# Performance work log

Measured on AMD Instinct MI355X. Metric: run time of the kernel, lower is better.

## Reference

```python
import jax, jax.numpy as jnp
import numpy as np

N_NODES = 50000
N_EDGES = 800000
N_GRAPHS = 128
ORIG_FEA = 92
NBR_FEA = 41
H = 64
N_CONV = 3
BN_EPS = 1e-5


def setup_inputs() -> dict:
    key = jax.random.key(0)
    ks = jax.random.split(key, 16)
    x = jax.random.normal(ks[0], (N_NODES, ORIG_FEA), dtype=jnp.float32)
    edge_attr = jax.random.normal(ks[1], (N_EDGES, NBR_FEA), dtype=jnp.float32)
    edge_index = jax.random.randint(ks[2], (2, N_EDGES), 0, N_NODES)
    batch = jnp.sort(jax.random.randint(ks[3], (N_NODES,), 0, N_GRAPHS))
    s_emb1 = 1.0 / np.sqrt(ORIG_FEA)
    s_emb2 = 1.0 / np.sqrt(NBR_FEA)
    s_conv = 1.0 / np.sqrt(3 * H)
    s_h = 1.0 / np.sqrt(H)
    return {
        "x": x,
        "edge_attr": edge_attr,
        "edge_index": edge_index,
        "batch": batch,
        "W_emb1": jax.random.uniform(ks[4], (ORIG_FEA, H), jnp.float32, -s_emb1, s_emb1),
        "b_emb1": jnp.zeros((H,), jnp.float32),
        "W_emb2": jax.random.uniform(ks[5], (NBR_FEA, H), jnp.float32, -s_emb2, s_emb2),
        "b_emb2": jnp.zeros((H,), jnp.float32),
        "Wf": jax.random.uniform(ks[6], (N_CONV, 3 * H, H), jnp.float32, -s_conv, s_conv),
        "bf": jnp.zeros((N_CONV, H), jnp.float32),
        "Ws": jax.random.uniform(ks[7], (N_CONV, 3 * H, H), jnp.float32, -s_conv, s_conv),
        "bs": jnp.zeros((N_CONV, H), jnp.float32),
        "gamma": jnp.ones((N_CONV, H), jnp.float32),
        "beta": jnp.zeros((N_CONV, H), jnp.float32),
        "W1": jax.random.uniform(ks[8], (H, H), jnp.float32, -s_h, s_h),
        "b1": jnp.zeros((H,), jnp.float32),
        "W2": jax.random.uniform(ks[9], (H, H), jnp.float32, -s_h, s_h),
        "b2": jnp.zeros((H,), jnp.float32),
        "Wo": jax.random.uniform(ks[10], (H, 1), jnp.float32, -s_h, s_h),
        "bo": jnp.zeros((1,), jnp.float32),
    }


def _batch_norm(h, g, b):
    # training-mode BatchNorm1d: biased batch statistics
    mu = jnp.mean(h, axis=0)
    var = jnp.var(h, axis=0)
    return (h - mu) * jax.lax.rsqrt(var + BN_EPS) * g + b


def reference(x, edge_attr, edge_index, batch, W_emb1, b_emb1, W_emb2, b_emb2,
              Wf, bf, Ws, bs, gamma, beta, W1, b1, W2, b2, Wo, bo):
    src = edge_index[0]  # x_j (source)
    dst = edge_index[1]  # x_i (target, aggregation index)
    h = x @ W_emb1 + b_emb1              # [N, H]
    e = edge_attr @ W_emb2 + b_emb2      # [E, H]
    for a in range(N_CONV):
        # CGConv: z_ij = [x_i, x_j, e_ij]; msg = sigmoid(lin_f(z)) * softplus(lin_s(z))
        z = jnp.concatenate([h[dst], h[src], e], axis=1)       # [E, 3H]
        msg = jax.nn.sigmoid(z @ Wf[a] + bf[a]) * jax.nn.softplus(z @ Ws[a] + bs[a])
        h = h + jax.ops.segment_sum(msg, dst, num_segments=N_NODES)
        h = _batch_norm(h, gamma[a], beta[a])
        if a != N_CONV - 1:
            h = jax.nn.relu(h)
        # dropout ratio is 0 -> no-op
    # JK='last' -> node representation is final h; mean pooling per graph
    sums = jax.ops.segment_sum(h, batch, num_segments=N_GRAPHS)              # [G, H]
    cnts = jax.ops.segment_sum(jnp.ones((N_NODES,), h.dtype), batch, num_segments=N_GRAPHS)
    y = sums / jnp.maximum(cnts, 1.0)[:, None]
    y = jax.nn.softplus(y @ W1 + b1)
    y = jax.nn.softplus(y @ W2 + b2)
    y = (y @ Wo + bo).squeeze(-1)  # [G]
    return y
```

## Files before the change

### kernel.cpp

```cpp
#include <hip/hip_runtime.h>
#include <hip/hip_bf16.h>
#include <math.h>

#define N_NODES 50000
#define N_EDGES 800000
#define N_GRAPHS 128
#define ORIG_FEA 92
#define NBR_FEA 41
#define H 64
#define N_CONV 3
#define BN_EPS 1e-5f

typedef float v2f __attribute__((ext_vector_type(2)));

__device__ __forceinline__ float sigmoidf_(float x) {
    return __fdividef(1.f, 1.f + __expf(-x));
}
__device__ __forceinline__ float softplusf_(float x) {
    return fmaxf(x, 0.f) + __logf(1.f + __expf(-fabsf(x)));
}

__global__ __launch_bounds__(256) void fold_kernel(
    const float* __restrict__ W_emb2, const float* __restrict__ b_emb2,
    const float* __restrict__ Wf, const float* __restrict__ bf,
    const float* __restrict__ Ws, const float* __restrict__ bs,
    float* __restrict__ W2c, float* __restrict__ cfs) {
    int a = blockIdx.x >> 1, gate = blockIdx.x & 1;
    const float* W = (gate ? Ws : Wf) + a * 192 * H + 128 * H;
    const float* bias = (gate ? bs : bf) + a * H;
    float* Wout = W2c + a * NBR_FEA * 2 * H;
    float* cout = cfs + a * 2 * H;
    for (int idx = threadIdx.x; idx < NBR_FEA * H; idx += blockDim.x) {
        int k = idx / H, j = idx % H;
        float acc = 0.f;
        for (int m = 0; m < H; ++m) acc += W_emb2[k * H + m] * W[m * H + j];
        Wout[k * 2 * H + 2 * j + gate] = acc;
    }
    for (int j = threadIdx.x; j < H; j += blockDim.x) {
        float acc = bias[j];
        for (int m = 0; m < H; ++m) acc += b_emb2[m] * W[m * H + j];
        cout[2 * j + gate] = acc;
    }
}

__global__ __launch_bounds__(256) void embed_kernel(
    const float* __restrict__ x, const float* __restrict__ W,
    const float* __restrict__ b, float* __restrict__ h) {
    __shared__ float lw[ORIG_FEA * H];
    for (int i = threadIdx.x; i < ORIG_FEA * H; i += blockDim.x) lw[i] = W[i];
    __syncthreads();
    int lane = threadIdx.x & 63;
    int wid = (blockIdx.x * blockDim.x + threadIdx.x) >> 6;
    int nw = (gridDim.x * blockDim.x) >> 6;
    for (int n = wid; n < N_NODES; n += nw) {
        int nu = __builtin_amdgcn_readfirstlane(n);
        const float* xr = x + (size_t)nu * ORIG_FEA;
        float acc = b[lane];
#pragma unroll
        for (int k = 0; k < ORIG_FEA; ++k) acc += xr[k] * lw[k * H + lane];
        h[(size_t)nu * H + lane] = acc;
    }
}

__global__ __launch_bounds__(256) void node_proj_kernel(
    const float* __restrict__ h,
    const float* __restrict__ Wf, const float* __restrict__ Ws,
    float* __restrict__ NPi, float* __restrict__ NPj,
    float* __restrict__ hsum) {
    __shared__ float lw[4 * H * H];
    for (int i = threadIdx.x; i < H * H; i += blockDim.x) {
        lw[i] = Wf[i];
        lw[H * H + i] = Wf[H * H + i];
        lw[2 * H * H + i] = Ws[i];
        lw[3 * H * H + i] = Ws[H * H + i];
    }
    __syncthreads();
    int lane = threadIdx.x & 63;
    int wid = (blockIdx.x * blockDim.x + threadIdx.x) >> 6;
    int nw = (gridDim.x * blockDim.x) >> 6;
    for (int n = wid; n < N_NODES; n += nw) {
        int nu = __builtin_amdgcn_readfirstlane(n);
        const float* hr = h + (size_t)nu * H;
        float pf = 0.f, qf = 0.f, ps = 0.f, qs = 0.f;
#pragma unroll
        for (int k = 0; k < H; ++k) {
            float s = hr[k];
            pf += s * lw[k * H + lane];
            qf += s * lw[H * H + k * H + lane];
            ps += s * lw[2 * H * H + k * H + lane];
            qs += s * lw[3 * H * H + k * H + lane];
        }
        v2f pi; pi.x = pf; pi.y = ps;
        v2f pj; pj.x = qf; pj.y = qs;
        *(v2f*)&NPi[(size_t)nu * 2 * H + 2 * lane] = pi;
        *(v2f*)&NPj[(size_t)nu * 2 * H + 2 * lane] = pj;
        hsum[(size_t)nu * H + lane] = hr[lane];
    }
}

__global__ __launch_bounds__(256, 2) void edge_kernel(
    const int* __restrict__ ei, const float* __restrict__ ea,
    const float* __restrict__ NPi, const float* __restrict__ NPj,
    const float* __restrict__ W2c, const float* __restrict__ cfs,
    float* __restrict__ hsum) {
    int lane = threadIdx.x & 63;
    v2f w[NBR_FEA];
#pragma unroll
    for (int k = 0; k < NBR_FEA; ++k)
        w[k] = *(const v2f*)&W2c[k * 2 * H + 2 * lane];
    v2f c2 = *(const v2f*)&cfs[2 * lane];
#pragma unroll
    for (int k = 0; k < NBR_FEA; ++k) asm volatile("" : "+v"(w[k]));
    int wid = (blockIdx.x * blockDim.x + threadIdx.x) >> 6;
    int nw = (gridDim.x * blockDim.x) >> 6;
    for (int e = wid; e < N_EDGES; e += nw) {
        int eu = __builtin_amdgcn_readfirstlane(e);
        int src = ei[eu];
        int dst = ei[N_EDGES + eu];
        v2f pi = *(const v2f*)&NPi[(size_t)dst * 2 * H + 2 * lane];
        v2f pj = *(const v2f*)&NPj[(size_t)src * 2 * H + 2 * lane];
        v2f acc = c2 + pi + pj;
        const float* er = ea + (size_t)eu * NBR_FEA;
#pragma unroll
        for (int k = 0; k < NBR_FEA; ++k) acc += w[k] * er[k];
        float msg = sigmoidf_(acc.x) * softplusf_(acc.y);
        atomicAdd(&hsum[(size_t)dst * H + lane], msg);
    }
}

__global__ __launch_bounds__(256) void bn_stats_kernel(
    const float* __restrict__ hsum, float* __restrict__ stats) {
    int lane = threadIdx.x & 63;
    int wl = threadIdx.x >> 6;
    int wid = (blockIdx.x * blockDim.x + threadIdx.x) >> 6;
    int nw = (gridDim.x * blockDim.x) >> 6;
    float s = 0.f, s2 = 0.f;
    for (int n = wid; n < N_NODES; n += nw) {
        float v = hsum[(size_t)n * H + lane];
        s += v;
        s2 += v * v;
    }
    __shared__ float ls[4 * 2 * H];
    ls[wl * 2 * H + lane] = s;
    ls[wl * 2 * H + H + lane] = s2;
    __syncthreads();
    if (wl == 0) {
        float a = ls[lane] + ls[2 * H + lane] + ls[4 * H + lane] + ls[6 * H + lane];
        float b = ls[H + lane] + ls[3 * H + lane] + ls[5 * H + lane] + ls[7 * H + lane];
        atomicAdd(&stats[lane], a);
        atomicAdd(&stats[H + lane], b);
    }
}

__global__ __launch_bounds__(256) void bn_apply_kernel(
    const float* __restrict__ hsum, const float* __restrict__ stats,
    const float* __restrict__ gamma, const float* __restrict__ beta,
    float* __restrict__ h, int relu) {
    int idx0 = blockIdx.x * blockDim.x + threadIdx.x;
    int stride = gridDim.x * blockDim.x;
    const float inv_n = 1.f / (float)N_NODES;
    for (int idx = idx0; idx < N_NODES * H; idx += stride) {
        int j = idx & (H - 1);
        float mu = stats[j] * inv_n;
        float var = stats[H + j] * inv_n - mu * mu;
        float inv = rsqrtf(var + BN_EPS);
        float v = (hsum[idx] - mu) * inv * gamma[j] + beta[j];
        if (relu) v = fmaxf(v, 0.f);
        h[idx] = v;
    }
}

__global__ __launch_bounds__(256) void pool_kernel(
    const float* __restrict__ h, const int* __restrict__ batch,
    float* __restrict__ gsum, float* __restrict__ gcnt) {
    int lane = threadIdx.x & 63;
    int wid = (blockIdx.x * blockDim.x + threadIdx.x) >> 6;
    int nw = (gridDim.x * blockDim.x) >> 6;
    for (int n = wid; n < N_NODES; n += nw) {
        int nu = __builtin_amdgcn_readfirstlane(n);
        int g = batch[nu];
        atomicAdd(&gsum[(size_t)g * H + lane], h[(size_t)nu * H + lane]);
        if (lane == 0) atomicAdd(&gcnt[g], 1.f);
    }
}

__global__ __launch_bounds__(64) void mlp_kernel(
    const float* __restrict__ gsum, const float* __restrict__ gcnt,
    const float* __restrict__ W1, const float* __restrict__ b1,
    const float* __restrict__ W2, const float* __restrict__ b2,
    const float* __restrict__ Wo, const float* __restrict__ bo,
    float* __restrict__ out) {
    int g = blockIdx.x;
    int lane = threadIdx.x;
    __shared__ float y[H];
    float cnt = fmaxf(gcnt[g], 1.f);
    y[lane] = gsum[(size_t)g * H + lane] / cnt;
    __syncthreads();
    float acc = b1[lane];
#pragma unroll
    for (int k = 0; k < H; ++k) acc += y[k] * W1[k * H + lane];
    float y1 = softplusf_(acc);
    __syncthreads();
    y[lane] = y1;
    __syncthreads();
    acc = b2[lane];
#pragma unroll
    for (int k = 0; k < H; ++k) acc += y[k] * W2[k * H + lane];
    float y2 = softplusf_(acc);
    float t = y2 * Wo[lane];
#pragma unroll
    for (int o = 32; o > 0; o >>= 1) t += __shfl_down(t, o, 64);
    if (lane == 0) out[g] = t + bo[0];
}

extern "C" void kernel_launch(void* const* d_in, const int* in_sizes, int n_in,
                              void* d_out, int out_size, void* d_ws, size_t ws_size,
                              hipStream_t stream) {
    const float* x = (const float*)d_in[0];
    const float* ea = (const float*)d_in[1];
    const int* ei = (const int*)d_in[2];
    const int* batch = (const int*)d_in[3];
    const float* W_emb1 = (const float*)d_in[4];
    const float* b_emb1 = (const float*)d_in[5];
    const float* W_emb2 = (const float*)d_in[6];
    const float* b_emb2 = (const float*)d_in[7];
    const float* Wf = (const float*)d_in[8];
    const float* bf = (const float*)d_in[9];
    const float* Ws = (const float*)d_in[10];
    const float* bs = (const float*)d_in[11];
    const float* gamma = (const float*)d_in[12];
    const float* beta = (const float*)d_in[13];
    const float* W1 = (const float*)d_in[14];
    const float* b1 = (const float*)d_in[15];
    const float* W2 = (const float*)d_in[16];
    const float* b2 = (const float*)d_in[17];
    const float* Wo = (const float*)d_in[18];
    const float* bo = (const float*)d_in[19];
    float* out = (float*)d_out;

    float* w = (float*)d_ws;
    float* stats = w;
    float* gsum = w + 3 * 2 * H;
    float* gcnt = gsum + N_GRAPHS * H;
    float* h = gcnt + N_GRAPHS;
    float* hsum = h + (size_t)N_NODES * H;
    float* NPi = hsum + (size_t)N_NODES * H;
    float* NPj = NPi + (size_t)N_NODES * 2 * H;
    float* W2c = NPj + (size_t)N_NODES * 2 * H;
    float* cfs = W2c + 3 * NBR_FEA * 2 * H;

    hipMemsetAsync(w, 0, (3 * 2 * H + N_GRAPHS * H + N_GRAPHS) * sizeof(float), stream);

    fold_kernel<<<6, 256, 0, stream>>>(W_emb2, b_emb2, Wf, bf, Ws, bs, W2c, cfs);
    embed_kernel<<<512, 256, 0, stream>>>(x, W_emb1, b_emb1, h);

    for (int a = 0; a < N_CONV; ++a) {
        node_proj_kernel<<<512, 256, 0, stream>>>(h, Wf + a * 192 * H, Ws + a * 192 * H,
                                                  NPi, NPj, hsum);
        edge_kernel<<<2048, 256, 0, stream>>>(ei, ea, NPi, NPj,
                                              W2c + a * NBR_FEA * 2 * H,
                                              cfs + a * 2 * H, hsum);
        bn_stats_kernel<<<256, 256, 0, stream>>>(hsum, stats + a * 2 * H);
        bn_apply_kernel<<<2048, 256, 0, stream>>>(hsum, stats + a * 2 * H,
                                                  gamma + a * H, beta + a * H, h,
                                                  a != N_CONV - 1 ? 1 : 0);
    }

    pool_kernel<<<784, 256, 0, stream>>>(h, batch, gsum, gcnt);
    mlp_kernel<<<128, 64, 0, stream>>>(gsum, gcnt, W1, b1, W2, b2, Wo, bo, out);
}
```

Measured before the change: 1.233 ms.

## Build CSR by destination and aggregate edges per node without atomics, fusing BN

```diff
diff --git a/kernel.cpp b/kernel.cpp
--- a/kernel.cpp
+++ b/kernel.cpp
@@ -45,7 +45,7 @@
 
 __global__ __launch_bounds__(256) void embed_kernel(
     const float* __restrict__ x, const float* __restrict__ W,
-    const float* __restrict__ b, float* __restrict__ h) {
+    const float* __restrict__ b, float* __restrict__ state) {
     __shared__ float lw[ORIG_FEA * H];
     for (int i = threadIdx.x; i < ORIG_FEA * H; i += blockDim.x) lw[i] = W[i];
     __syncthreads();
@@ -58,33 +58,90 @@
         float acc = b[lane];
 #pragma unroll
         for (int k = 0; k < ORIG_FEA; ++k) acc += xr[k] * lw[k * H + lane];
-        h[(size_t)nu * H + lane] = acc;
-    }
-}
-
-__global__ __launch_bounds__(256) void node_proj_kernel(
-    const float* __restrict__ h,
+        state[(size_t)nu * H + lane] = acc;
+    }
+}
+
+__global__ __launch_bounds__(256) void hist_kernel(
+    const int* __restrict__ ei, int* __restrict__ deg) {
+    int e = blockIdx.x * blockDim.x + threadIdx.x;
+    if (e < N_EDGES) atomicAdd(&deg[ei[N_EDGES + e]], 1);
+}
+
+__global__ __launch_bounds__(256) void scan_kernel(
+    const int* __restrict__ deg, int* __restrict__ off, int* __restrict__ cur) {
+    __shared__ int part[256];
+    const int CH = (N_NODES + 255) / 256;
+    int t = threadIdx.x;
+    int lo = t * CH, hi = min(lo + CH, N_NODES);
+    int s = 0;
+    for (int i = lo; i < hi; ++i) s += deg[i];
+    part[t] = s;
+    __syncthreads();
+    for (int o = 1; o < 256; o <<= 1) {
+        int v = (t >= o) ? part[t - o] : 0;
+        __syncthreads();
+        part[t] += v;
+        __syncthreads();
+    }
+    int run = (t == 0) ? 0 : part[t - 1];
+    for (int i = lo; i < hi; ++i) {
+        off[i] = run;
+        cur[i] = run;
+        run += deg[i];
+    }
+    if (t == 255) off[N_NODES] = run;
+}
+
+__global__ __launch_bounds__(256) void scatter_kernel(
+    const int* __restrict__ ei, int* __restrict__ cur,
+    int* __restrict__ perm, int* __restrict__ src_s) {
+    int e = blockIdx.x * blockDim.x + threadIdx.x;
+    if (e < N_EDGES) {
+        int d = ei[N_EDGES + e];
+        int p = atomicAdd(&cur[d], 1);
+        perm[p] = e;
+        src_s[p] = ei[e];
+    }
+}
+
+__global__ __launch_bounds__(256) void node_proj_bn_kernel(
+    const float* __restrict__ state, const float* __restrict__ stats,
+    const float* __restrict__ gamma, const float* __restrict__ beta,
     const float* __restrict__ Wf, const float* __restrict__ Ws,
     float* __restrict__ NPi, float* __restrict__ NPj,
-    float* __restrict__ hsum) {
+    float* __restrict__ hres, int mode) {
     __shared__ float lw[4 * H * H];
+    __shared__ float slot[4][H];
     for (int i = threadIdx.x; i < H * H; i += blockDim.x) {
         lw[i] = Wf[i];
         lw[H * H + i] = Wf[H * H + i];
         lw[2 * H * H + i] = Ws[i];
         lw[3 * H * H + i] = Ws[H * H + i];
     }
-    __syncthreads();
     int lane = threadIdx.x & 63;
+    int wl = threadIdx.x >> 6;
+    float A = 1.f, B = 0.f;
+    if (mode) {
+        const float inv_n = 1.f / (float)N_NODES;
+        float mu = stats[lane] * inv_n;
+        float var = stats[H + lane] * inv_n - mu * mu;
+        float inv = rsqrtf(var + BN_EPS);
+        A = inv * gamma[lane];
+        B = beta[lane] - mu * A;
+    }
+    __syncthreads();
     int wid = (blockIdx.x * blockDim.x + threadIdx.x) >> 6;
     int nw = (gridDim.x * blockDim.x) >> 6;
     for (int n = wid; n < N_NODES; n += nw) {
-        int nu = __builtin_amdgcn_readfirstlane(n);
-        const float* hr = h + (size_t)nu * H;
+        float z = state[(size_t)n * H + lane];
+        float hn = mode ? fmaxf(z * A + B, 0.f) : z;
+        hres[(size_t)n * H + lane] = hn;
+        slot[wl][lane] = hn;
         float pf = 0.f, qf = 0.f, ps = 0.f, qs = 0.f;
 #pragma unroll
         for (int k = 0; k < H; ++k) {
-            float s = hr[k];
+            float s = slot[wl][k];
             pf += s * lw[k * H + lane];
             qf += s * lw[H * H + k * H + lane];
             ps += s * lw[2 * H * H + k * H + lane];
@@ -92,17 +149,18 @@
         }
         v2f pi; pi.x = pf; pi.y = ps;
         v2f pj; pj.x = qf; pj.y = qs;
-        *(v2f*)&NPi[(size_t)nu * 2 * H + 2 * lane] = pi;
-        *(v2f*)&NPj[(size_t)nu * 2 * H + 2 * lane] = pj;
-        hsum[(size_t)nu * H + lane] = hr[lane];
-    }
-}
-
-__global__ __launch_bounds__(256, 2) void edge_kernel(
-    const int* __restrict__ ei, const float* __restrict__ ea,
+        *(v2f*)&NPi[(size_t)n * 2 * H + 2 * lane] = pi;
+        *(v2f*)&NPj[(size_t)n * 2 * H + 2 * lane] = pj;
+    }
+}
+
+__global__ __launch_bounds__(256, 3) void edge_csr_kernel(
+    const int* __restrict__ off, const int* __restrict__ perm,
+    const int* __restrict__ src_s, const float* __restrict__ ea,
     const float* __restrict__ NPi, const float* __restrict__ NPj,
     const float* __restrict__ W2c, const float* __restrict__ cfs,
-    float* __restrict__ hsum) {
+    const float* __restrict__ hres, float* __restrict__ state,
+    float* __restrict__ stats) {
     int lane = threadIdx.x & 63;
     v2f w[NBR_FEA];
 #pragma unroll
@@ -110,76 +168,53 @@
         w[k] = *(const v2f*)&W2c[k * 2 * H + 2 * lane];
     v2f c2 = *(const v2f*)&cfs[2 * lane];
 #pragma unroll
-    for (int k = 0; k < NBR_FEA; ++k) asm volatile("" : "+v"(w[k]));
+    for (int k = 0; k < NBR_FEA; ++k)
+        asm volatile("" : "+v"(w[k])::"memory");
+    asm volatile("" : "+v"(c2)::"memory");
+    float s = 0.f, s2 = 0.f;
     int wid = (blockIdx.x * blockDim.x + threadIdx.x) >> 6;
     int nw = (gridDim.x * blockDim.x) >> 6;
-    for (int e = wid; e < N_EDGES; e += nw) {
-        int eu = __builtin_amdgcn_readfirstlane(e);
-        int src = ei[eu];
-        int dst = ei[N_EDGES + eu];
-        v2f pi = *(const v2f*)&NPi[(size_t)dst * 2 * H + 2 * lane];
-        v2f pj = *(const v2f*)&NPj[(size_t)src * 2 * H + 2 * lane];
-        v2f acc = c2 + pi + pj;
-        const float* er = ea + (size_t)eu * NBR_FEA;
-#pragma unroll
-        for (int k = 0; k < NBR_FEA; ++k) acc += w[k] * er[k];
-        float msg = sigmoidf_(acc.x) * softplusf_(acc.y);
-        atomicAdd(&hsum[(size_t)dst * H + lane], msg);
-    }
-}
-
-__global__ __launch_bounds__(256) void bn_stats_kernel(
-    const float* __restrict__ hsum, float* __restrict__ stats) {
+    for (int n = wid; n < N_NODES; n += nw) {
+        int nu = __builtin_amdgcn_readfirstlane(n);
+        float acc = hres[(size_t)nu * H + lane];
+        v2f base = c2 + *(const v2f*)&NPi[(size_t)nu * 2 * H + 2 * lane];
+        int e0 = off[nu], e1 = off[nu + 1];
+        for (int e = e0; e < e1; ++e) {
+            int eu = __builtin_amdgcn_readfirstlane(perm[e]);
+            int src = __builtin_amdgcn_readfirstlane(src_s[e]);
+            v2f a2 = base + *(const v2f*)&NPj[(size_t)src * 2 * H + 2 * lane];
+            const float* er = ea + (size_t)eu * NBR_FEA;
+#pragma unroll
+            for (int k = 0; k < NBR_FEA; ++k) a2 += w[k] * er[k];
+            acc += sigmoidf_(a2.x) * softplusf_(a2.y);
+        }
+        state[(size_t)nu * H + lane] = acc;
+        s += acc;
+        s2 += acc * acc;
+    }
+    atomicAdd(&stats[lane], s);
+    atomicAdd(&stats[H + lane], s2);
+}
+
+__global__ __launch_bounds__(256) void pool_bn_kernel(
+    const float* __restrict__ state, const float* __restrict__ stats,
+    const float* __restrict__ gamma, const float* __restrict__ beta,
+    const int* __restrict__ batch, float* __restrict__ gsum,
+    float* __restrict__ gcnt) {
     int lane = threadIdx.x & 63;
-    int wl = threadIdx.x >> 6;
-    int wid = (blockIdx.x * blockDim.x + threadIdx.x) >> 6;
-    int nw = (gridDim.x * blockDim.x) >> 6;
-    float s = 0.f, s2 = 0.f;
-    for (int n = wid; n < N_NODES; n += nw) {
-        float v = hsum[(size_t)n * H + lane];
-        s += v;
-        s2 += v * v;
-    }
-    __shared__ float ls[4 * 2 * H];
-    ls[wl * 2 * H + lane] = s;
-    ls[wl * 2 * H + H + lane] = s2;
-    __syncthreads();
-    if (wl == 0) {
-        float a = ls[lane] + ls[2 * H + lane] + ls[4 * H + lane] + ls[6 * H + lane];
-        float b = ls[H + lane] + ls[3 * H + lane] + ls[5 * H + lane] + ls[7 * H + lane];
-        atomicAdd(&stats[lane], a);
-        atomicAdd(&stats[H + lane], b);
-    }
-}
-
-__global__ __launch_bounds__(256) void bn_apply_kernel(
-    const float* __restrict__ hsum, const float* __restrict__ stats,
-    const float* __restrict__ gamma, const float* __restrict__ beta,
-    float* __restrict__ h, int relu) {
-    int idx0 = blockIdx.x * blockDim.x + threadIdx.x;
-    int stride = gridDim.x * blockDim.x;
     const float inv_n = 1.f / (float)N_NODES;
-    for (int idx = idx0; idx < N_NODES * H; idx += stride) {
-        int j = idx & (H - 1);
-        float mu = stats[j] * inv_n;
-        float var = stats[H + j] * inv_n - mu * mu;
-        float inv = rsqrtf(var + BN_EPS);
-        float v = (hsum[idx] - mu) * inv * gamma[j] + beta[j];
-        if (relu) v = fmaxf(v, 0.f);
-        h[idx] = v;
-    }
-}
-
-__global__ __launch_bounds__(256) void pool_kernel(
-    const float* __restrict__ h, const int* __restrict__ batch,
-    float* __restrict__ gsum, float* __restrict__ gcnt) {
-    int lane = threadIdx.x & 63;
+    float mu = stats[lane] * inv_n;
+    float var = stats[H + lane] * inv_n - mu * mu;
+    float inv = rsqrtf(var + BN_EPS);
+    float A = inv * gamma[lane];
+    float B = beta[lane] - mu * A;
     int wid = (blockIdx.x * blockDim.x + threadIdx.x) >> 6;
     int nw = (gridDim.x * blockDim.x) >> 6;
     for (int n = wid; n < N_NODES; n += nw) {
         int nu = __builtin_amdgcn_readfirstlane(n);
         int g = batch[nu];
-        atomicAdd(&gsum[(size_t)g * H + lane], h[(size_t)nu * H + lane]);
+        float v = state[(size_t)nu * H + lane] * A + B;
+        atomicAdd(&gsum[(size_t)g * H + lane], v);
         if (lane == 0) atomicAdd(&gcnt[g], 1.f);
     }
 }
@@ -240,32 +275,40 @@
 
     float* w = (float*)d_ws;
     float* stats = w;
-    float* gsum = w + 3 * 2 * H;
+    float* gsum = stats + 3 * 2 * H;
     float* gcnt = gsum + N_GRAPHS * H;
-    float* h = gcnt + N_GRAPHS;
-    float* hsum = h + (size_t)N_NODES * H;
-    float* NPi = hsum + (size_t)N_NODES * H;
+    int* deg = (int*)(gcnt + N_GRAPHS);
+    const size_t zero_elems = 3 * 2 * H + N_GRAPHS * H + N_GRAPHS + N_NODES;
+    int* off = deg + N_NODES;
+    int* cur = off + N_NODES + 1;
+    int* perm = cur + N_NODES;
+    int* src_s = perm + N_EDGES;
+    float* W2c = (float*)(src_s + N_EDGES);
+    float* cfs = W2c + 3 * NBR_FEA * 2 * H;
+    float* state = cfs + 3 * 2 * H;
+    float* hres = state + (size_t)N_NODES * H;
+    float* NPi = hres + (size_t)N_NODES * H;
     float* NPj = NPi + (size_t)N_NODES * 2 * H;
-    float* W2c = NPj + (size_t)N_NODES * 2 * H;
-    float* cfs = W2c + 3 * NBR_FEA * 2 * H;
-
-    hipMemsetAsync(w, 0, (3 * 2 * H + N_GRAPHS * H + N_GRAPHS) * sizeof(float), stream);
+
+    hipMemsetAsync(w, 0, zero_elems * sizeof(float), stream);
 
     fold_kernel<<<6, 256, 0, stream>>>(W_emb2, b_emb2, Wf, bf, Ws, bs, W2c, cfs);
-    embed_kernel<<<512, 256, 0, stream>>>(x, W_emb1, b_emb1, h);
+    embed_kernel<<<512, 256, 0, stream>>>(x, W_emb1, b_emb1, state);
+    hist_kernel<<<(N_EDGES + 255) / 256, 256, 0, stream>>>(ei, deg);
+    scan_kernel<<<1, 256, 0, stream>>>(deg, off, cur);
+    scatter_kernel<<<(N_EDGES + 255) / 256, 256, 0, stream>>>(ei, cur, perm, src_s);
 
     for (int a = 0; a < N_CONV; ++a) {
-        node_proj_kernel<<<512, 256, 0, stream>>>(h, Wf + a * 192 * H, Ws + a * 192 * H,
-                                                  NPi, NPj, hsum);
-        edge_kernel<<<2048, 256, 0, stream>>>(ei, ea, NPi, NPj,
-                                              W2c + a * NBR_FEA * 2 * H,
-                                              cfs + a * 2 * H, hsum);
-        bn_stats_kernel<<<256, 256, 0, stream>>>(hsum, stats + a * 2 * H);
-        bn_apply_kernel<<<2048, 256, 0, stream>>>(hsum, stats + a * 2 * H,
-                                                  gamma + a * H, beta + a * H, h,
-                                                  a != N_CONV - 1 ? 1 : 0);
-    }
-
-    pool_kernel<<<784, 256, 0, stream>>>(h, batch, gsum, gcnt);
+        node_proj_bn_kernel<<<512, 256, 0, stream>>>(
+            state, stats + (a - 1) * 2 * H, gamma + (a - 1) * H, beta + (a - 1) * H,
+            Wf + a * 192 * H, Ws + a * 192 * H, NPi, NPj, hres, a > 0 ? 1 : 0);
+        edge_csr_kernel<<<2048, 256, 0, stream>>>(
+            off, perm, src_s, ea, NPi, NPj, W2c + a * NBR_FEA * 2 * H,
+            cfs + a * 2 * H, hres, state, stats + a * 2 * H);
+    }
+
+    pool_bn_kernel<<<784, 256, 0, stream>>>(state, stats + 2 * 2 * H,
+                                            gamma + 2 * H, beta + 2 * H,
+                                            batch, gsum, gcnt);
     mlp_kernel<<<128, 64, 0, stream>>>(gsum, gcnt, W1, b1, W2, b2, Wo, bo, out);
 }
```

Result: slower. 1.615 ms (+31.0%).
